# Kernel optimization log

Hardware: AMD Instinct MI355X
Metric: run time of the kernel (lower is better)

Reference implementation:

```python
import jax, jax.numpy as jnp
import numpy as np

HIDDEN = 512
HEADS = 8
HEAD_DIM = HIDDEN // HEADS
MAX_DIST = 10
B, N = 16, 512
EPS = 1e-5


def _layer_norm(x, g, b):
    mu = jnp.mean(x, axis=-1, keepdims=True)
    var = jnp.mean(jnp.square(x - mu), axis=-1, keepdims=True)
    return (x - mu) * jax.lax.rsqrt(var + EPS) * g + b


def setup_inputs() -> dict:
    key = jax.random.key(0)
    ks = jax.random.split(key, 16)
    s = 0.02
    inp = {
        "x": jax.random.normal(ks[0], (B, N, HIDDEN), jnp.float32),
        "distances": jax.random.randint(ks[1], (B, N, N), 0, MAX_DIST, jnp.int32),
        "edge_features": jax.random.normal(ks[2], (B, N, N), jnp.float32),
        "attn_mask": jax.random.randint(ks[3], (B, N), 0, 2).astype(bool),
        "Wq": jax.random.normal(ks[4], (HIDDEN, HIDDEN), jnp.float32) * s,
        "bq": jnp.zeros((HIDDEN,), jnp.float32),
        "Wk": jax.random.normal(ks[5], (HIDDEN, HIDDEN), jnp.float32) * s,
        "bk": jnp.zeros((HIDDEN,), jnp.float32),
        "Wv": jax.random.normal(ks[6], (HIDDEN, HIDDEN), jnp.float32) * s,
        "bv": jnp.zeros((HIDDEN,), jnp.float32),
        "Wo": jax.random.normal(ks[7], (HIDDEN, HIDDEN), jnp.float32) * s,
        "bo": jnp.zeros((HIDDEN,), jnp.float32),
        "spatial_emb": jax.random.normal(ks[8], (MAX_DIST, HEADS), jnp.float32) * s,
        "edge_w": jax.random.normal(ks[9], (HEADS,), jnp.float32) * s,
        "edge_b": jnp.zeros((HEADS,), jnp.float32),
        "ln1_g": jnp.ones((HIDDEN,), jnp.float32),
        "ln1_b": jnp.zeros((HIDDEN,), jnp.float32),
        "ln2_g": jnp.ones((HIDDEN,), jnp.float32),
        "ln2_b": jnp.zeros((HIDDEN,), jnp.float32),
        "W1": jax.random.normal(ks[10], (HIDDEN, 4 * HIDDEN), jnp.float32) * s,
        "b1": jnp.zeros((4 * HIDDEN,), jnp.float32),
        "W2": jax.random.normal(ks[11], (4 * HIDDEN, HIDDEN), jnp.float32) * s,
        "b2": jnp.zeros((HIDDEN,), jnp.float32),
    }
    return inp


def reference(x, distances, edge_features, attn_mask, Wq, bq, Wk, bk, Wv, bv,
              Wo, bo, spatial_emb, edge_w, edge_b, ln1_g, ln1_b, ln2_g, ln2_b,
              W1, b1, W2, b2):
    b, n, _ = x.shape
    q = (x @ Wq + bq).reshape(b, n, HEADS, HEAD_DIM)
    k = (x @ Wk + bk).reshape(b, n, HEADS, HEAD_DIM)
    v = (x @ Wv + bv).reshape(b, n, HEADS, HEAD_DIM)
    # [b, h, i, j] attention scores
    scores = jnp.einsum('bihd,bjhd->bhij', q, k) / np.sqrt(HEAD_DIM).astype(np.float32)
    spatial_bias = spatial_emb[distances]                       # [b, i, j, h]
    edge_bias = edge_features[..., None] * edge_w + edge_b      # [b, i, j, h]
    scores = scores + jnp.transpose(spatial_bias + edge_bias, (0, 3, 1, 2))
    scores = jnp.where(attn_mask[:, None, None, :], -jnp.inf, scores)
    attn = jax.nn.softmax(scores, axis=-1)
    out = jnp.einsum('bhij,bjhd->bihd', attn, v).reshape(b, n, HIDDEN)
    out = out @ Wo + bo
    h = _layer_norm(x + out, ln1_g, ln1_b)
    ffn = jax.nn.relu(h @ W1 + b1) @ W2 + b2
    return _layer_norm(h + ffn, ln2_g, ln2_b)
```

## Files before the change

kernel.cpp:

```cpp
#include <hip/hip_runtime.h>
#include <stdint.h>
#include <stddef.h>

#define SEQ   512
#define HID   512
#define NHEAD 8
#define HD    64
#define NBATCH 16
#define NTOK  8192
#define MAXD  10
#define LOG2E 1.4426950408889634f

typedef __attribute__((ext_vector_type(8))) short short8;
typedef __attribute__((ext_vector_type(4))) float f32x4;

typedef __attribute__((address_space(3))) void        as3_void;
typedef const __attribute__((address_space(1))) void  as1_cvoid;

#define MFMA16(a,b,c) __builtin_amdgcn_mfma_f32_16x16x32_bf16((a),(b),(c),0,0,0)

__device__ __forceinline__ float bf2f(uint16_t u){ return __uint_as_float(((uint32_t)u)<<16); }
__device__ __forceinline__ uint16_t f2bf(float f){
  uint32_t i = __float_as_uint(f);
  return (uint16_t)((i + 0x7fffu + ((i>>16)&1u)) >> 16);
}

enum { EPI_BF16=0, EPI_F32=3, EPI_RELU=4 };

__global__ __launch_bounds__(256) void f2bf_kernel(
    const float* __restrict__ in, uint16_t* __restrict__ out, int n4)
{
  int i = blockIdx.x*256 + threadIdx.x;
  if (i < n4){
    float4 v = *(const float4*)(in + (size_t)i*4);
    *(ushort4*)(out + (size_t)i*4) =
        make_ushort4(f2bf(v.x), f2bf(v.y), f2bf(v.z), f2bf(v.w));
  }
}

__global__ __launch_bounds__(256) void transpose_all(
    const float* __restrict__ Wq, const float* __restrict__ Wk,
    const float* __restrict__ Wv, const float* __restrict__ Wo,
    const float* __restrict__ W1, const float* __restrict__ W2,
    uint16_t* __restrict__ tq, uint16_t* __restrict__ tk,
    uint16_t* __restrict__ tv, uint16_t* __restrict__ to_,
    uint16_t* __restrict__ t1, uint16_t* __restrict__ t2)
{
  __shared__ uint16_t tile[32][33];
  int id = blockIdx.x;
  const float* in; uint16_t* out; int R, C, tx, ty;
  if (id < 1024) {
    int m = id >> 8, loc = id & 255;
    in  = (m==0)?Wq:(m==1)?Wk:(m==2)?Wv:Wo;
    out = (m==0)?tq:(m==1)?tk:(m==2)?tv:to_;
    R = 512; C = 512; ty = loc>>4; tx = loc&15;
  } else if (id < 2048) {
    int loc = id-1024; in=W1; out=t1; R=512; C=2048; ty=loc>>6; tx=loc&63;
  } else {
    int loc = id-2048; in=W2; out=t2; R=2048; C=512; ty=loc>>4; tx=loc&15;
  }
  int bx = tx*32, by = ty*32;
  int lx = threadIdx.x & 31, ly = threadIdx.x >> 5;
  #pragma unroll
  for (int i=ly; i<32; i+=8) tile[i][lx] = f2bf(in[(size_t)(by+i)*C + bx+lx]);
  __syncthreads();
  #pragma unroll
  for (int i=ly; i<32; i+=8) out[(size_t)(bx+i)*R + by+lx] = tile[lx][i];
}

__global__ __launch_bounds__(512) void pack_bias(
    const int*   __restrict__ dist,
    const float* __restrict__ edge,
    const int*   __restrict__ mask,
    uint32_t*    __restrict__ outp)
{
  __shared__ int   dl[16][260];
  __shared__ float el[16][260];
  __shared__ int   ml[512];
  const int b  = blockIdx.y;
  const int it = blockIdx.x;
  const int t  = threadIdx.x;
  ml[t] = mask[b*SEQ + t];

  #pragma unroll
  for (int jh=0; jh<2; ++jh){
    if (jh) __syncthreads();
    {
      const int r  = t >> 5;
      const int c0 = (t & 31) * 8;
      const size_t g = ((size_t)b*SEQ + it*16 + r)*SEQ + jh*256 + c0;
      *(int4*)&dl[r][c0]     = *(const int4*)&dist[g];
      *(int4*)&dl[r][c0+4]   = *(const int4*)&dist[g+4];
      *(float4*)&el[r][c0]   = *(const float4*)&edge[g];
      *(float4*)&el[r][c0+4] = *(const float4*)&edge[g+4];
    }
    __syncthreads();
    {
      const int i   = t & 15;
      const int j0p = (t >> 4) * 8;
      const int jt  = jh*4 + (j0p >> 6);
      const int jn  = (j0p >> 4) & 3;
      const int lg  = (j0p & 15) >> 2;
      uint32_t w[8];
      #pragma unroll
      for (int e=0; e<8; ++e){
        const int jl = j0p + e;
        const int jg = jh*256 + jl;
        const uint32_t d  = (uint32_t)dl[i][jl] & 0xFFu;
        const uint32_t mk = (ml[jg] ? 1u : 0u) << 8;
        w[e] = ((uint32_t)f2bf(el[i][jl]) << 16) | mk | d;
      }
      uint32_t* ob = outp + ((((size_t)b*32 + it)*8 + jt)*64)*16;
      const int lane0 = lg*16 + i, lane1 = (lg+1)*16 + i;
      *(uint4*)&ob[lane0*16 + jn*4] = make_uint4(w[0],w[1],w[2],w[3]);
      *(uint4*)&ob[lane1*16 + jn*4] = make_uint4(w[4],w[5],w[6],w[7]);
    }
  }
}

template<int BM, int BN>
__device__ __forceinline__ void gemm_tile_mainloop(
    const uint16_t* __restrict__ A, const uint16_t* __restrict__ Bt,
    int K, int m0, int n0, uint16_t* lA, uint16_t* lB,
    f32x4 acc[4][(BM==128)?4:((BN==128)?2:1)])
{
  constexpr int NJ  = (BM==128)?4:((BN==128)?2:1);
  constexpr int ARD = BM/32;
  constexpr int BRD = BN/32;
  constexpr bool DB = (BM==64) && (BN==64);
  const int t = threadIdx.x;
  const int w = t>>6, l = t&63;
  const int lg = l>>4, lc = l&15;
  const int wr = (BM==128)?(w>>1):0;
  const int wc = (BM==128)?(w&1):w;
  const int swz = lc & 7;
  const int kSteps = K>>6;

  auto stage = [&](int kt, int buf){
    const int k0 = kt<<6;
    #pragma unroll
    for (int rd=0; rd<ARD; ++rd){
      const int e   = rd*2048 + t*8;
      const int row = e>>6;
      const int col = (((e>>3)&7) ^ (row&7))*8;
      const uint16_t* ga = A + (size_t)(m0+row)*K + (k0+col);
      char* la = (char*)(lA + buf*(BM*64)) + rd*4096 + w*1024;
      __builtin_amdgcn_global_load_lds((as1_cvoid*)ga, (as3_void*)la, 16, 0, 0);
    }
    #pragma unroll
    for (int rd=0; rd<BRD; ++rd){
      const int e   = rd*2048 + t*8;
      const int row = e>>6;
      const int col = (((e>>3)&7) ^ (row&7))*8;
      const uint16_t* gb = Bt + (size_t)(n0+row)*K + (k0+col);
      char* lb = (char*)(lB + buf*(BN*64)) + rd*4096 + w*1024;
      __builtin_amdgcn_global_load_lds((as1_cvoid*)gb, (as3_void*)lb, 16, 0, 0);
    }
  };

  auto compute = [&](const uint16_t* rA, const uint16_t* rB){
    #pragma unroll
    for (int kk=0; kk<2; ++kk){
      const int cc = (kk*4 + lg) ^ swz;
      short8 af[4], bfr[NJ];
      #pragma unroll
      for (int i=0;i<4;i++)
        af[i]  = *(const short8*)&rA[(wr*64 + i*16 + lc)*64 + cc*8];
      #pragma unroll
      for (int j=0;j<NJ;j++)
        bfr[j] = *(const short8*)&rB[(wc*16*NJ + j*16 + lc)*64 + cc*8];
      #pragma unroll
      for (int i=0;i<4;i++)
        #pragma unroll
        for (int j=0;j<NJ;j++)
          acc[i][j] = MFMA16(af[i], bfr[j], acc[i][j]);
    }
  };

  if constexpr (DB){
    stage(0, 0);
    __syncthreads();
    int cur = 0;
    for (int kt=0; kt<kSteps; ++kt){
      if (kt+1 < kSteps) stage(kt+1, cur^1);
      compute(lA + cur*(BM*64), lB + cur*(BN*64));
      __syncthreads();
      cur ^= 1;
    }
  } else {
    for (int kt=0; kt<kSteps; ++kt){
      stage(kt, 0);
      __syncthreads();
      compute(lA, lB);
      __syncthreads();
    }
  }
}

template<int EPI, int BM, int BN>
__global__ __launch_bounds__(256,2) void gemm_bt(
    const uint16_t* __restrict__ A, const uint16_t* __restrict__ Bt,
    const float* __restrict__ bias, void* __restrict__ outp,
    int M, int N, int K)
{
  constexpr int NJ = (BM==128)?4:((BN==128)?2:1);
  constexpr int NB = ((BM==64)&&(BN==64)) ? 2 : 1;
  __shared__ uint16_t lA[NB*BM*64];
  __shared__ uint16_t lB[NB*BN*64];
  f32x4 acc[4][NJ];
  #pragma unroll
  for (int i=0;i<4;i++)
    #pragma unroll
    for (int j=0;j<NJ;j++){ f32x4 z = {0.f,0.f,0.f,0.f}; acc[i][j]=z; }
  const int m0 = blockIdx.x*BM, n0 = blockIdx.y*BN;
  gemm_tile_mainloop<BM,BN>(A, Bt, K, m0, n0, lA, lB, acc);

  const int t=threadIdx.x, w=t>>6, l=t&63, lg=l>>4, lc=l&15;
  const int wr=(BM==128)?(w>>1):0, wc=(BM==128)?(w&1):w;
  #pragma unroll
  for (int j=0;j<NJ;j++){
    const int col = n0 + wc*16*NJ + j*16 + lc;
    const float bs = bias[col];
    #pragma unroll
    for (int i=0;i<4;i++){
      const int rowb = m0 + wr*64 + i*16 + lg*4;
      #pragma unroll
      for (int r=0;r<4;r++){
        float v = acc[i][j][r] + bs;
        if constexpr (EPI==EPI_RELU)   v = fmaxf(v, 0.f);
        if constexpr (EPI==EPI_F32)
          ((float*)outp)[(size_t)(rowb+r)*N + col] = v;
        else
          ((uint16_t*)outp)[(size_t)(rowb+r)*N + col] = f2bf(v);
      }
    }
  }
}

__global__ __launch_bounds__(256,2) void qkv_gemm(
    const uint16_t* __restrict__ x,
    const uint16_t* __restrict__ wtq, const uint16_t* __restrict__ wtk,
    const uint16_t* __restrict__ wtv,
    const float* __restrict__ bq, const float* __restrict__ bk,
    const float* __restrict__ bv,
    uint16_t* __restrict__ qo, uint16_t* __restrict__ kp,
    uint16_t* __restrict__ vp)
{
  __shared__ uint16_t lA[128*64];
  __shared__ uint16_t lB[128*64];
  const int z = blockIdx.z;
  const uint16_t* Bt = (z==0)?wtq:(z==1)?wtk:wtv;
  const float*  bias = (z==0)?bq :(z==1)?bk :bv;
  f32x4 acc[4][4];
  #pragma unroll
  for (int i=0;i<4;i++)
    #pragma unroll
    for (int j=0;j<4;j++){ f32x4 zz = {0.f,0.f,0.f,0.f}; acc[i][j]=zz; }
  const int m0 = blockIdx.x*128, n0 = blockIdx.y*128;
  gemm_tile_mainloop<128,128>(x, Bt, HID, m0, n0, lA, lB, acc);

  const int t=threadIdx.x, w=t>>6, l=t&63, lg=l>>4, lc=l&15, wr=w>>1, wc=w&1;
  if (z==0){
    const float scale = 0.125f * LOG2E;
    #pragma unroll
    for (int j=0;j<4;j++){
      const int col = n0 + wc*64 + j*16 + lc;
      const float bs = bias[col];
      #pragma unroll
      for (int i=0;i<4;i++){
        const int rowb = m0 + wr*64 + i*16 + lg*4;
        #pragma unroll
        for (int r=0;r<4;r++)
          qo[(size_t)(rowb+r)*HID + col] = f2bf((acc[i][j][r] + bs)*scale);
      }
    }
  } else if (z==1){
    #pragma unroll
    for (int j=0;j<4;j++){
      const int col = n0 + wc*64 + j*16 + lc;
      const float bs = bias[col];
      const int h_ = col>>6, cm = col&63, kk = cm>>5, lgk = (cm>>3)&3, e = col&7;
      #pragma unroll
      for (int i=0;i<4;i++){
        const int rowb = m0 + wr*64 + i*16 + lg*4;
        #pragma unroll
        for (int r=0;r<4;r++){
          const int tok = rowb + r;
          const int b_ = tok>>9, tl = tok&511;
          const int jt = tl>>6, jn = (tl>>4)&3, lck = tl&15;
          kp[((((size_t)(b_*8+h_)*8 + jt)*4 + jn)*2 + kk)*512
             + (lgk*16 + lck)*8 + e] = f2bf(acc[i][j][r] + bs);
        }
      }
    }
  } else {
    #pragma unroll
    for (int j=0;j<4;j++){
      const int col = n0 + wc*64 + j*16 + lc;
      const float bs = bias[col];
      const int h_ = col>>6, dn = (col>>4)&3, lcv = col&15;
      #pragma unroll
      for (int i=0;i<4;i++){
        const int rowb = m0 + wr*64 + i*16 + lg*4;
        const int b_ = rowb>>9, tl = rowb&511;
        const int jt = tl>>6, kk = (tl>>5)&1, lgv = (tl>>3)&3, e0 = tl&7;
        *(ushort4*)&vp[((((size_t)(b_*8+h_)*8 + jt)*2 + kk)*4 + dn)*512
                       + (lgv*16 + lcv)*8 + e0] =
            make_ushort4(f2bf(acc[i][j][0]+bs), f2bf(acc[i][j][1]+bs),
                         f2bf(acc[i][j][2]+bs), f2bf(acc[i][j][3]+bs));
      }
    }
  }
}

__global__ __launch_bounds__(512,4) void attn_kernel(
    const uint16_t* __restrict__ q,
    const uint16_t* __restrict__ kp,
    const uint16_t* __restrict__ vp,
    const uint32_t* __restrict__ biasp,
    const float*    __restrict__ semb,
    const float*    __restrict__ ew,
    const float*    __restrict__ eb,
    uint16_t* __restrict__ out)
{
  __shared__ float sp_rep[NHEAD][32][11];
  __shared__ uint16_t plds[NHEAD][2][16*64];
  const int b  = blockIdx.y;
  const int it = blockIdx.x;
  const int i0 = it*16;
  const int t  = threadIdx.x;
  const int h  = t>>6, l = t&63, lg = l>>4, lc = l&15;
  for (int i = t; i < NHEAD*32*MAXD; i += 512){
    const int hh = i / (32*MAXD), rem = i % (32*MAXD);
    const int a = rem / MAXD, d = rem % MAXD;
    sp_rep[hh][a][d] = (semb[d*NHEAD + hh] + eb[hh]) * LOG2E;
  }
  __syncthreads();
  const float ewf = ew[h] * LOG2E;
  const float* spl = &sp_rep[h][l&31][0];
  char* pbase = (char*)&plds[h][0][0];
  const int swz = (lc&7)<<4;

  short8 qf[2];
  #pragma unroll
  for (int kk=0;kk<2;kk++)
    qf[kk] = *(const short8*)&q[(size_t)(b*SEQ + i0 + lc)*HID + h*HD + kk*32 + lg*8];

  const uint4* bp = (const uint4*)(biasp + (((size_t)b*32 + it)*8)*64*16);
  const uint16_t* kpb = kp + (size_t)(b*8+h)*8*4*2*512 + l*8;
  const uint16_t* vpb = vp + (size_t)(b*8+h)*8*2*4*512 + l*8;

  float mrun[2] = {-1e30f, -1e30f};
  float lrun[2] = {0.f, 0.f};
  f32x4 oacc[2][4];
  #pragma unroll
  for (int s=0;s<2;s++)
    #pragma unroll
    for (int dn=0;dn<4;dn++){ f32x4 z={0.f,0.f,0.f,0.f}; oacc[s][dn]=z; }

  #pragma unroll
  for (int p=0; p<4; ++p){
    #pragma unroll
    for (int s=0; s<2; ++s){
      const int jt = s*4 + p;
      uint32_t uw[16];
      {
        const uint4* bq_ = bp + (jt*64 + l)*4;
        *(uint4*)&uw[0]  = bq_[0];
        *(uint4*)&uw[4]  = bq_[1];
        *(uint4*)&uw[8]  = bq_[2];
        *(uint4*)&uw[12] = bq_[3];
      }
      f32x4 st[4];
      #pragma unroll
      for (int jn=0;jn<4;jn++){ f32x4 z={0.f,0.f,0.f,0.f}; st[jn]=z; }
      __builtin_amdgcn_s_setprio(1);
      #pragma unroll
      for (int jn=0;jn<4;jn++){
        #pragma unroll
        for (int kk=0;kk<2;kk++){
          short8 kf = *(const short8*)&kpb[(size_t)((jt*4 + jn)*2 + kk)*512];
          st[jn] = MFMA16(kf, qf[kk], st[jn]);
        }
      }
      __builtin_amdgcn_s_setprio(0);
      float tmax = -1e30f;
      #pragma unroll
      for (int jn=0;jn<4;jn++){
        #pragma unroll
        for (int r=0;r<4;r++){
          const uint32_t u = uw[jn*4+r];
          float sv = st[jn][r] + spl[u & 0xFFu]
                   + bf2f((uint16_t)(u >> 16))*ewf;
          if (u & 0x100u) sv = -1e30f;
          st[jn][r] = sv;
          tmax = fmaxf(tmax, sv);
        }
      }
      {
        float tm = fmaxf(tmax, __shfl_xor(tmax, 16, 64));
        tm = fmaxf(tm, __shfl_xor(tm, 32, 64));
        float mnew = fmaxf(mrun[s], tm);
        mnew = fmaxf(mnew, -1e20f);
        const float c = __builtin_amdgcn_exp2f(mrun[s] - mnew);
        mrun[s] = mnew;
        float lsum = 0.f;
        char* pb = pbase + s*(16*64*2) + lc*128;
        #pragma unroll
        for (int jn=0;jn<4;jn++){
          float p0 = __builtin_amdgcn_exp2f(st[jn][0]-mnew);
          float p1 = __builtin_amdgcn_exp2f(st[jn][1]-mnew);
          float p2 = __builtin_amdgcn_exp2f(st[jn][2]-mnew);
          float p3 = __builtin_amdgcn_exp2f(st[jn][3]-mnew);
          lsum += (p0+p1)+(p2+p3);
          *(ushort4*)(pb + (((jn*16 + lg*4)*2) ^ swz)) =
              make_ushort4(f2bf(p0), f2bf(p1), f2bf(p2), f2bf(p3));
        }
        lrun[s] = lrun[s]*c + lsum;
        #pragma unroll
        for (int r=0;r<4;r++){
          const float cr = __shfl(c, lg*4+r, 64);
          #pragma unroll
          for (int dn=0;dn<4;dn++) oacc[s][dn][r] *= cr;
        }
      }
    }
    #pragma unroll
    for (int s=0; s<2; ++s){
      const int jt = s*4 + p;
      char* pb = pbase + s*(16*64*2) + lc*128;
      __builtin_amdgcn_s_setprio(1);
      #pragma unroll
      for (int kk=0;kk<2;kk++){
        short8 pa = *(const short8*)(pb + (((kk*32 + lg*8)*2) ^ swz));
        #pragma unroll
        for (int dn=0;dn<4;dn++){
          short8 vb = *(const short8*)&vpb[(size_t)((jt*2 + kk)*4 + dn)*512];
          oacc[s][dn] = MFMA16(pa, vb, oacc[s][dn]);
        }
      }
      __builtin_amdgcn_s_setprio(0);
    }
  }
  {
    const float mm = fmaxf(mrun[0], mrun[1]);
    const float c0 = __builtin_amdgcn_exp2f(mrun[0]-mm);
    const float c1 = __builtin_amdgcn_exp2f(mrun[1]-mm);
    float ls = lrun[0]*c0 + lrun[1]*c1;
    ls += __shfl_xor(ls, 16, 64);
    ls += __shfl_xor(ls, 32, 64);
    const float inv = 1.f/ls;
    #pragma unroll
    for (int r=0;r<4;r++){
      const float cr0 = __shfl(c0, lg*4+r, 64);
      const float cr1 = __shfl(c1, lg*4+r, 64);
      const float ir  = __shfl(inv, lg*4+r, 64);
      const size_t orow = ((size_t)b*SEQ + i0 + lg*4 + r)*HID;
      #pragma unroll
      for (int dn=0;dn<4;dn++)
        out[orow + h*HD + dn*16 + lc] =
            f2bf((oacc[0][dn][r]*cr0 + oacc[1][dn][r]*cr1)*ir);
    }
  }
}

__global__ __launch_bounds__(256) void ln_kernel(
    const float* __restrict__ a, const float* __restrict__ bsrc,
    const float* __restrict__ g, const float* __restrict__ bb,
    float* __restrict__ of, uint16_t* __restrict__ ob)
{
  const int row = blockIdx.x*4 + (threadIdx.x>>6);
  const int l = threadIdx.x & 63;
  const float* ar = a    + (size_t)row*HID;
  const float* br = bsrc + (size_t)row*HID;
  float u[8];
  {
    float4 a0 = *(const float4*)(ar + l*4);
    float4 a1 = *(const float4*)(ar + 256 + l*4);
    float4 b0 = *(const float4*)(br + l*4);
    float4 b1 = *(const float4*)(br + 256 + l*4);
    u[0]=a0.x+b0.x; u[1]=a0.y+b0.y; u[2]=a0.z+b0.z; u[3]=a0.w+b0.w;
    u[4]=a1.x+b1.x; u[5]=a1.y+b1.y; u[6]=a1.z+b1.z; u[7]=a1.w+b1.w;
  }
  float s=0.f, ss=0.f;
  #pragma unroll
  for (int e=0;e<8;e++){ s += u[e]; ss += u[e]*u[e]; }
  #pragma unroll
  for (int off=32; off>=1; off>>=1){
    s  += __shfl_xor(s,  off, 64);
    ss += __shfl_xor(ss, off, 64);
  }
  const float mu  = s*(1.f/512.f);
  const float inv = rsqrtf(ss*(1.f/512.f) - mu*mu + 1e-5f);
  float y[8];
  #pragma unroll
  for (int e=0;e<4;e++){
    int c0 = l*4+e, c1 = 256+l*4+e;
    y[e]   = (u[e]  -mu)*inv*g[c0] + bb[c0];
    y[4+e] = (u[4+e]-mu)*inv*g[c1] + bb[c1];
  }
  if (of){
    float* orow = of + (size_t)row*HID;
    *(float4*)(orow + l*4)       = make_float4(y[0],y[1],y[2],y[3]);
    *(float4*)(orow + 256 + l*4) = make_float4(y[4],y[5],y[6],y[7]);
  }
  if (ob){
    uint16_t* brow = ob + (size_t)row*HID;
    *(ushort4*)(brow + l*4)       = make_ushort4(f2bf(y[0]),f2bf(y[1]),f2bf(y[2]),f2bf(y[3]));
    *(ushort4*)(brow + 256 + l*4) = make_ushort4(f2bf(y[4]),f2bf(y[5]),f2bf(y[6]),f2bf(y[7]));
  }
}

extern "C" void kernel_launch(void* const* d_in, const int* in_sizes, int n_in,
                              void* d_out, int out_size, void* d_ws, size_t ws_size,
                              hipStream_t stream)
{
  (void)in_sizes; (void)n_in; (void)out_size; (void)ws_size;
  const float* x    = (const float*)d_in[0];
  const int*   dist = (const int*)  d_in[1];
  const float* edge = (const float*)d_in[2];
  const int*   mask = (const int*)  d_in[3];
  const float* Wq = (const float*)d_in[4];
  const float* bq = (const float*)d_in[5];
  const float* Wk = (const float*)d_in[6];
  const float* bk = (const float*)d_in[7];
  const float* Wv = (const float*)d_in[8];
  const float* bv = (const float*)d_in[9];
  const float* Wo = (const float*)d_in[10];
  const float* bo = (const float*)d_in[11];
  const float* semb = (const float*)d_in[12];
  const float* ew   = (const float*)d_in[13];
  const float* eb   = (const float*)d_in[14];
  const float* ln1g = (const float*)d_in[15];
  const float* ln1b = (const float*)d_in[16];
  const float* ln2g = (const float*)d_in[17];
  const float* ln2b = (const float*)d_in[18];
  const float* W1 = (const float*)d_in[19];
  const float* b1 = (const float*)d_in[20];
  const float* W2 = (const float*)d_in[21];
  const float* b2 = (const float*)d_in[22];

  char* ws = (char*)d_ws;
  uint16_t* xb16  = (uint16_t*)ws;
  uint16_t* qbuf  = xb16  + (size_t)NTOK*HID;
  uint16_t* kpbuf = qbuf  + (size_t)NTOK*HID;
  uint16_t* vpbuf = kpbuf + (size_t)NTOK*HID;
  uint16_t* aobuf = vpbuf + (size_t)NTOK*HID;
  uint16_t* f1buf = qbuf;
  uint32_t* biasp = (uint32_t*)(ws + (size_t)5*NTOK*HID*2);
  float*    tbuf  = (float*)biasp;
  float*    t2buf = tbuf;
  float*    hbuf  = tbuf + (size_t)NTOK*HID;
  uint16_t* hb16  = (uint16_t*)(hbuf + (size_t)NTOK*HID);
  uint16_t* wt    = hb16 + (size_t)NTOK*HID;
  uint16_t* wtq = wt;
  uint16_t* wtk = wtq + 512*512;
  uint16_t* wtv = wtk + 512*512;
  uint16_t* wto = wtv + 512*512;
  uint16_t* wt1 = wto + 512*512;
  uint16_t* wt2 = wt1 + 512*2048;

  pack_bias<<<dim3(32,16), 512, 0, stream>>>(dist, edge, mask, biasp);

  transpose_all<<<3072, 256, 0, stream>>>(Wq,Wk,Wv,Wo,W1,W2, wtq,wtk,wtv,wto,wt1,wt2);

  f2bf_kernel<<<4096, 256, 0, stream>>>(x, xb16, NTOK*HID/4);

  qkv_gemm<<<dim3(64,4,3), 256, 0, stream>>>(xb16, wtq,wtk,wtv, bq,bk,bv,
                                             qbuf, kpbuf, vpbuf);

  attn_kernel<<<dim3(32,16), 512, 0, stream>>>(qbuf, kpbuf, vpbuf, biasp,
                                               semb, ew, eb, aobuf);

  gemm_bt<EPI_F32,64,64><<<dim3(128,8), 256, 0, stream>>>(aobuf, wto, bo, tbuf, NTOK, HID, HID);

  ln_kernel<<<2048, 256, 0, stream>>>(tbuf, x, ln1g, ln1b, hbuf, hb16);

  gemm_bt<EPI_RELU,128,128><<<dim3(64,16), 256, 0, stream>>>(hb16, wt1, b1, f1buf, NTOK, 2048, HID);

  gemm_bt<EPI_F32,64,64><<<dim3(128,8), 256, 0, stream>>>(f1buf, wt2, b2, t2buf, NTOK, HID, 2048);

  ln_kernel<<<2048, 256, 0, stream>>>(t2buf, hbuf, ln2g, ln2b, (float*)d_out, nullptr);
}
```

Baseline: 162.0 us.

## Shrink GEMM tiles, emit bf16 residual intermediates, pad attention P buffer

The QKV and FFN1 GEMMs move from 128x128 to 64x64 tiles with larger grids. The output-projection and FFN2 GEMMs now write bf16 instead of fp32, and the layer-norm kernel reads bf16 with contiguous 8-element vectors. In the attention kernel, the XOR swizzle on the P staging buffer is replaced by row padding to 72 elements. These changes aim to raise parallelism and cut intermediate memory traffic, at the cost of less data reuse per tile and reduced precision of the pre-LN sums.

```diff
diff --git a/kernel.cpp b/kernel.cpp
--- a/kernel.cpp
+++ b/kernel.cpp
@@ -246,69 +246,56 @@
     uint16_t* __restrict__ qo, uint16_t* __restrict__ kp,
     uint16_t* __restrict__ vp)
 {
-  __shared__ uint16_t lA[128*64];
-  __shared__ uint16_t lB[128*64];
+  __shared__ uint16_t lA[2*64*64];
+  __shared__ uint16_t lB[2*64*64];
   const int z = blockIdx.z;
   const uint16_t* Bt = (z==0)?wtq:(z==1)?wtk:wtv;
   const float*  bias = (z==0)?bq :(z==1)?bk :bv;
-  f32x4 acc[4][4];
-  #pragma unroll
-  for (int i=0;i<4;i++)
-    #pragma unroll
-    for (int j=0;j<4;j++){ f32x4 zz = {0.f,0.f,0.f,0.f}; acc[i][j]=zz; }
-  const int m0 = blockIdx.x*128, n0 = blockIdx.y*128;
-  gemm_tile_mainloop<128,128>(x, Bt, HID, m0, n0, lA, lB, acc);
-
-  const int t=threadIdx.x, w=t>>6, l=t&63, lg=l>>4, lc=l&15, wr=w>>1, wc=w&1;
+  f32x4 acc[4][1];
+  #pragma unroll
+  for (int i=0;i<4;i++){ f32x4 zz = {0.f,0.f,0.f,0.f}; acc[i][0]=zz; }
+  const int m0 = blockIdx.x*64, n0 = blockIdx.y*64;
+  gemm_tile_mainloop<64,64>(x, Bt, HID, m0, n0, lA, lB, acc);
+
+  const int t=threadIdx.x, w=t>>6, l=t&63, lg=l>>4, lc=l&15;
+  const int col = n0 + w*16 + lc;
   if (z==0){
     const float scale = 0.125f * LOG2E;
-    #pragma unroll
-    for (int j=0;j<4;j++){
-      const int col = n0 + wc*64 + j*16 + lc;
-      const float bs = bias[col];
-      #pragma unroll
-      for (int i=0;i<4;i++){
-        const int rowb = m0 + wr*64 + i*16 + lg*4;
-        #pragma unroll
-        for (int r=0;r<4;r++)
-          qo[(size_t)(rowb+r)*HID + col] = f2bf((acc[i][j][r] + bs)*scale);
-      }
+    const float bs = bias[col];
+    #pragma unroll
+    for (int i=0;i<4;i++){
+      const int rowb = m0 + i*16 + lg*4;
+      #pragma unroll
+      for (int r=0;r<4;r++)
+        qo[(size_t)(rowb+r)*HID + col] = f2bf((acc[i][0][r] + bs)*scale);
     }
   } else if (z==1){
-    #pragma unroll
-    for (int j=0;j<4;j++){
-      const int col = n0 + wc*64 + j*16 + lc;
-      const float bs = bias[col];
-      const int h_ = col>>6, cm = col&63, kk = cm>>5, lgk = (cm>>3)&3, e = col&7;
-      #pragma unroll
-      for (int i=0;i<4;i++){
-        const int rowb = m0 + wr*64 + i*16 + lg*4;
-        #pragma unroll
-        for (int r=0;r<4;r++){
-          const int tok = rowb + r;
-          const int b_ = tok>>9, tl = tok&511;
-          const int jt = tl>>6, jn = (tl>>4)&3, lck = tl&15;
-          kp[((((size_t)(b_*8+h_)*8 + jt)*4 + jn)*2 + kk)*512
-             + (lgk*16 + lck)*8 + e] = f2bf(acc[i][j][r] + bs);
-        }
+    const float bs = bias[col];
+    const int h_ = col>>6, cm = col&63, kk = cm>>5, lgk = (cm>>3)&3, e = col&7;
+    #pragma unroll
+    for (int i=0;i<4;i++){
+      const int rowb = m0 + i*16 + lg*4;
+      #pragma unroll
+      for (int r=0;r<4;r++){
+        const int tok = rowb + r;
+        const int b_ = tok>>9, tl = tok&511;
+        const int jt = tl>>6, jn = (tl>>4)&3, lck = tl&15;
+        kp[((((size_t)(b_*8+h_)*8 + jt)*4 + jn)*2 + kk)*512
+           + (lgk*16 + lck)*8 + e] = f2bf(acc[i][0][r] + bs);
       }
     }
   } else {
-    #pragma unroll
-    for (int j=0;j<4;j++){
-      const int col = n0 + wc*64 + j*16 + lc;
-      const float bs = bias[col];
-      const int h_ = col>>6, dn = (col>>4)&3, lcv = col&15;
-      #pragma unroll
-      for (int i=0;i<4;i++){
-        const int rowb = m0 + wr*64 + i*16 + lg*4;
-        const int b_ = rowb>>9, tl = rowb&511;
-        const int jt = tl>>6, kk = (tl>>5)&1, lgv = (tl>>3)&3, e0 = tl&7;
-        *(ushort4*)&vp[((((size_t)(b_*8+h_)*8 + jt)*2 + kk)*4 + dn)*512
-                       + (lgv*16 + lcv)*8 + e0] =
-            make_ushort4(f2bf(acc[i][j][0]+bs), f2bf(acc[i][j][1]+bs),
-                         f2bf(acc[i][j][2]+bs), f2bf(acc[i][j][3]+bs));
-      }
+    const float bs = bias[col];
+    const int h_ = col>>6, dn = (col>>4)&3, lcv = col&15;
+    #pragma unroll
+    for (int i=0;i<4;i++){
+      const int rowb = m0 + i*16 + lg*4;
+      const int b_ = rowb>>9, tl = rowb&511;
+      const int jt = tl>>6, kk = (tl>>5)&1, lgv = (tl>>3)&3, e0 = tl&7;
+      *(ushort4*)&vp[((((size_t)(b_*8+h_)*8 + jt)*2 + kk)*4 + dn)*512
+                     + (lgv*16 + lcv)*8 + e0] =
+          make_ushort4(f2bf(acc[i][0][0]+bs), f2bf(acc[i][0][1]+bs),
+                       f2bf(acc[i][0][2]+bs), f2bf(acc[i][0][3]+bs));
     }
   }
 }
@@ -324,7 +311,7 @@
     uint16_t* __restrict__ out)
 {
   __shared__ float sp_rep[NHEAD][32][11];
-  __shared__ uint16_t plds[NHEAD][2][16*64];
+  __shared__ uint16_t plds[NHEAD][2][16*72];
   const int b  = blockIdx.y;
   const int it = blockIdx.x;
   const int i0 = it*16;
@@ -338,8 +325,7 @@
   __syncthreads();
   const float ewf = ew[h] * LOG2E;
   const float* spl = &sp_rep[h][l&31][0];
-  char* pbase = (char*)&plds[h][0][0];
-  const int swz = (lc&7)<<4;
+  char* pbase = (char*)&plds[h][0][0] + lc*144;
 
   short8 qf[2];
   #pragma unroll
@@ -405,7 +391,7 @@
         const float c = __builtin_amdgcn_exp2f(mrun[s] - mnew);
         mrun[s] = mnew;
         float lsum = 0.f;
-        char* pb = pbase + s*(16*64*2) + lc*128;
+        char* pb = pbase + s*(16*72*2);
         #pragma unroll
         for (int jn=0;jn<4;jn++){
           float p0 = __builtin_amdgcn_exp2f(st[jn][0]-mnew);
@@ -413,7 +399,7 @@
           float p2 = __builtin_amdgcn_exp2f(st[jn][2]-mnew);
           float p3 = __builtin_amdgcn_exp2f(st[jn][3]-mnew);
           lsum += (p0+p1)+(p2+p3);
-          *(ushort4*)(pb + (((jn*16 + lg*4)*2) ^ swz)) =
+          *(ushort4*)(pb + (jn*16 + lg*4)*2) =
               make_ushort4(f2bf(p0), f2bf(p1), f2bf(p2), f2bf(p3));
         }
         lrun[s] = lrun[s]*c + lsum;
@@ -428,11 +414,11 @@
     #pragma unroll
     for (int s=0; s<2; ++s){
       const int jt = s*4 + p;
-      char* pb = pbase + s*(16*64*2) + lc*128;
+      char* pb = pbase + s*(16*72*2);
       __builtin_amdgcn_s_setprio(1);
       #pragma unroll
       for (int kk=0;kk<2;kk++){
-        short8 pa = *(const short8*)(pb + (((kk*32 + lg*8)*2) ^ swz));
+        short8 pa = *(const short8*)(pb + (kk*32 + lg*8)*2);
         #pragma unroll
         for (int dn=0;dn<4;dn++){
           short8 vb = *(const short8*)&vpb[(size_t)((jt*2 + kk)*4 + dn)*512];
@@ -465,23 +451,23 @@
 }
 
 __global__ __launch_bounds__(256) void ln_kernel(
-    const float* __restrict__ a, const float* __restrict__ bsrc,
+    const uint16_t* __restrict__ a, const float* __restrict__ bsrc,
     const float* __restrict__ g, const float* __restrict__ bb,
     float* __restrict__ of, uint16_t* __restrict__ ob)
 {
   const int row = blockIdx.x*4 + (threadIdx.x>>6);
   const int l = threadIdx.x & 63;
-  const float* ar = a    + (size_t)row*HID;
-  const float* br = bsrc + (size_t)row*HID;
+  const int c0 = l*8;
+  const uint16_t* ar = a    + (size_t)row*HID + c0;
+  const float*    br = bsrc + (size_t)row*HID + c0;
+  short8 av = *(const short8*)ar;
+  float4 b0 = *(const float4*)br;
+  float4 b1 = *(const float4*)(br+4);
   float u[8];
-  {
-    float4 a0 = *(const float4*)(ar + l*4);
-    float4 a1 = *(const float4*)(ar + 256 + l*4);
-    float4 b0 = *(const float4*)(br + l*4);
-    float4 b1 = *(const float4*)(br + 256 + l*4);
-    u[0]=a0.x+b0.x; u[1]=a0.y+b0.y; u[2]=a0.z+b0.z; u[3]=a0.w+b0.w;
-    u[4]=a1.x+b1.x; u[5]=a1.y+b1.y; u[6]=a1.z+b1.z; u[7]=a1.w+b1.w;
-  }
+  u[0]=bf2f((uint16_t)av[0])+b0.x; u[1]=bf2f((uint16_t)av[1])+b0.y;
+  u[2]=bf2f((uint16_t)av[2])+b0.z; u[3]=bf2f((uint16_t)av[3])+b0.w;
+  u[4]=bf2f((uint16_t)av[4])+b1.x; u[5]=bf2f((uint16_t)av[5])+b1.y;
+  u[6]=bf2f((uint16_t)av[6])+b1.z; u[7]=bf2f((uint16_t)av[7])+b1.w;
   float s=0.f, ss=0.f;
   #pragma unroll
   for (int e=0;e<8;e++){ s += u[e]; ss += u[e]*u[e]; }
@@ -492,22 +478,22 @@
   }
   const float mu  = s*(1.f/512.f);
   const float inv = rsqrtf(ss*(1.f/512.f) - mu*mu + 1e-5f);
+  float4 g0 = *(const float4*)(g + c0),  g1 = *(const float4*)(g + c0 + 4);
+  float4 q0 = *(const float4*)(bb + c0), q1 = *(const float4*)(bb + c0 + 4);
   float y[8];
-  #pragma unroll
-  for (int e=0;e<4;e++){
-    int c0 = l*4+e, c1 = 256+l*4+e;
-    y[e]   = (u[e]  -mu)*inv*g[c0] + bb[c0];
-    y[4+e] = (u[4+e]-mu)*inv*g[c1] + bb[c1];
-  }
+  y[0]=(u[0]-mu)*inv*g0.x+q0.x; y[1]=(u[1]-mu)*inv*g0.y+q0.y;
+  y[2]=(u[2]-mu)*inv*g0.z+q0.z; y[3]=(u[3]-mu)*inv*g0.w+q0.w;
+  y[4]=(u[4]-mu)*inv*g1.x+q1.x; y[5]=(u[5]-mu)*inv*g1.y+q1.y;
+  y[6]=(u[6]-mu)*inv*g1.z+q1.z; y[7]=(u[7]-mu)*inv*g1.w+q1.w;
   if (of){
-    float* orow = of + (size_t)row*HID;
-    *(float4*)(orow + l*4)       = make_float4(y[0],y[1],y[2],y[3]);
-    *(float4*)(orow + 256 + l*4) = make_float4(y[4],y[5],y[6],y[7]);
+    float* orow = of + (size_t)row*HID + c0;
+    *(float4*)orow     = make_float4(y[0],y[1],y[2],y[3]);
+    *(float4*)(orow+4) = make_float4(y[4],y[5],y[6],y[7]);
   }
   if (ob){
-    uint16_t* brow = ob + (size_t)row*HID;
-    *(ushort4*)(brow + l*4)       = make_ushort4(f2bf(y[0]),f2bf(y[1]),f2bf(y[2]),f2bf(y[3]));
-    *(ushort4*)(brow + 256 + l*4) = make_ushort4(f2bf(y[4]),f2bf(y[5]),f2bf(y[6]),f2bf(y[7]));
+    uint16_t* brow = ob + (size_t)row*HID + c0;
+    *(ushort4*)brow     = make_ushort4(f2bf(y[0]),f2bf(y[1]),f2bf(y[2]),f2bf(y[3]));
+    *(ushort4*)(brow+4) = make_ushort4(f2bf(y[4]),f2bf(y[5]),f2bf(y[6]),f2bf(y[7]));
   }
 }
 
@@ -548,9 +534,9 @@
   uint16_t* aobuf = vpbuf + (size_t)NTOK*HID;
   uint16_t* f1buf = qbuf;
   uint32_t* biasp = (uint32_t*)(ws + (size_t)5*NTOK*HID*2);
-  float*    tbuf  = (float*)biasp;
-  float*    t2buf = tbuf;
-  float*    hbuf  = tbuf + (size_t)NTOK*HID;
+  uint16_t* tb16  = (uint16_t*)biasp;
+  uint16_t* t2b16 = tb16;
+  float*    hbuf  = (float*)((char*)biasp + (size_t)NTOK*HID*4);
   uint16_t* hb16  = (uint16_t*)(hbuf + (size_t)NTOK*HID);
   uint16_t* wt    = hb16 + (size_t)NTOK*HID;
   uint16_t* wtq = wt;
@@ -566,19 +552,19 @@
 
   f2bf_kernel<<<4096, 256, 0, stream>>>(x, xb16, NTOK*HID/4);
 
-  qkv_gemm<<<dim3(64,4,3), 256, 0, stream>>>(xb16, wtq,wtk,wtv, bq,bk,bv,
-                                             qbuf, kpbuf, vpbuf);
+  qkv_gemm<<<dim3(128,8,3), 256, 0, stream>>>(xb16, wtq,wtk,wtv, bq,bk,bv,
+                                              qbuf, kpbuf, vpbuf);
 
   attn_kernel<<<dim3(32,16), 512, 0, stream>>>(qbuf, kpbuf, vpbuf, biasp,
                                                semb, ew, eb, aobuf);
 
-  gemm_bt<EPI_F32,64,64><<<dim3(128,8), 256, 0, stream>>>(aobuf, wto, bo, tbuf, NTOK, HID, HID);
-
-  ln_kernel<<<2048, 256, 0, stream>>>(tbuf, x, ln1g, ln1b, hbuf, hb16);
-
-  gemm_bt<EPI_RELU,128,128><<<dim3(64,16), 256, 0, stream>>>(hb16, wt1, b1, f1buf, NTOK, 2048, HID);
-
-  gemm_bt<EPI_F32,64,64><<<dim3(128,8), 256, 0, stream>>>(f1buf, wt2, b2, t2buf, NTOK, HID, 2048);
-
-  ln_kernel<<<2048, 256, 0, stream>>>(t2buf, hbuf, ln2g, ln2b, (float*)d_out, nullptr);
-}
+  gemm_bt<EPI_BF16,64,64><<<dim3(128,8), 256, 0, stream>>>(aobuf, wto, bo, tb16, NTOK, HID, HID);
+
+  ln_kernel<<<2048, 256, 0, stream>>>(tb16, x, ln1g, ln1b, hbuf, hb16);
+
+  gemm_bt<EPI_RELU,64,64><<<dim3(128,32), 256, 0, stream>>>(hb16, wt1, b1, f1buf, NTOK, 2048, HID);
+
+  gemm_bt<EPI_BF16,64,64><<<dim3(128,8), 256, 0, stream>>>(f1buf, wt2, b2, t2b16, NTOK, HID, 2048);
+
+  ln_kernel<<<2048, 256, 0, stream>>>(t2b16, hbuf, ln2g, ln2b, (float*)d_out, nullptr);
+}
```

After: 171.6 us. 1.06x slower.
